# Performance work log

Measured on AMD Instinct MI355X. Metric: run time of the kernel, lower is better.

## Reference

```python
import jax, jax.numpy as jnp
import numpy as np

LENS = 4.0
SCALE = 0.25
NUM_HEADS = 16


def _multispike(u):
    # floor(clamp(u, 0, 4) + 0.5)
    return jnp.floor(jnp.clip(u, 0.0, 4.0) + 0.5)


def _ms_act(x):
    # Multispike module: spike(4*x) / 4
    return _multispike(4.0 * x) / 4.0


def setup_inputs() -> dict:
    key = jax.random.key(0)
    ks = jax.random.split(key, 5)
    N, D = 65536, 1024
    x = jax.random.normal(ks[0], (N, D), dtype=jnp.float32)
    s = 1.0 / np.sqrt(D)
    Wq = jax.random.normal(ks[1], (D, D), dtype=jnp.float32) * s
    Wk = jax.random.normal(ks[2], (D, D), dtype=jnp.float32) * s
    Wv = jax.random.normal(ks[3], (D, D), dtype=jnp.float32) * s
    Wp = jax.random.normal(ks[4], (D, D), dtype=jnp.float32) * s
    return {"x": x, "Wq": Wq, "Wk": Wk, "Wv": Wv, "Wp": Wp}


def reference(x, Wq, Wk, Wv, Wp):
    N, C = x.shape
    H = NUM_HEADS
    hd = C // H

    xs = _ms_act(x)
    q = _ms_act(xs @ Wq.T)  # [N, C]
    k = _ms_act(xs @ Wk.T)
    v = _ms_act(xs @ Wv.T)

    q = q.reshape(N, H, hd)
    k = k.reshape(N, H, hd)
    v = v.reshape(N, H, hd)

    # linear attention: kv = k^T @ v per head -> [H, hd, hd]
    kv = jnp.einsum('nhd,nhe->hde', k, v)
    attn = jnp.einsum('nhd,hde->nhe', q, kv) * SCALE  # [N, H, hd]
    attn = attn.reshape(N, C)
    return attn @ Wp.T
```

## Files before the change

kernel.cpp:

```cpp
#include <hip/hip_runtime.h>
#include <stdint.h>


typedef __attribute__((ext_vector_type(8))) __bf16 bf16x8;
typedef __attribute__((ext_vector_type(4))) float f32x4;

__device__ __forceinline__ float bf2f(unsigned short u) {
  return __builtin_bit_cast(float, (unsigned int)u << 16);
}
__device__ __forceinline__ unsigned short f2bf(float f) {
  unsigned int u = __builtin_bit_cast(unsigned int, f);
  u += 0x7FFFu + ((u >> 16) & 1u);
  return (unsigned short)(u >> 16);
}
__device__ __forceinline__ float ms_act(float x) {
  float t = fminf(fmaxf(4.0f * x, 0.0f), 4.0f);
  return floorf(t + 0.5f) * 0.25f;
}

#define GLD16(g, l)                                                                           \
  __builtin_amdgcn_global_load_lds((__attribute__((address_space(1))) void*)(const void*)(g), \
                                   (__attribute__((address_space(3))) void*)(l), 16, 0, 0)

__global__ __launch_bounds__(256) void split_w_kernel(
    const float* __restrict__ Wq, const float* __restrict__ Wk, const float* __restrict__ Wv,
    unsigned short* __restrict__ Whi, unsigned short* __restrict__ Wlo, float* __restrict__ kv) {
  const int tid = threadIdx.x;
  const int w = blockIdx.y;
  const float* W = (w == 0) ? Wq : (w == 1) ? Wk : Wv;
  const size_t base = (size_t)w * 1048576u;
  const size_t i = (size_t)(blockIdx.x * 256 + tid) * 4;
  float4 v = *(const float4*)&W[i];
  float vv[4] = {v.x, v.y, v.z, v.w};
  unsigned short h4[4], l4[4];
#pragma unroll
  for (int j = 0; j < 4; ++j) {
    unsigned short hi = f2bf(vv[j]);
    h4[j] = hi;
    l4[j] = f2bf(vv[j] - bf2f(hi));
  }
  *(uint2*)&Whi[base + i] = make_uint2((unsigned)h4[0] | ((unsigned)h4[1] << 16),
                                       (unsigned)h4[2] | ((unsigned)h4[3] << 16));
  *(uint2*)&Wlo[base + i] = make_uint2((unsigned)l4[0] | ((unsigned)l4[1] << 16),
                                       (unsigned)l4[2] | ((unsigned)l4[3] << 16));
  if (w == 0 && blockIdx.x < 64) {
    ((float4*)kv)[blockIdx.x * 256 + tid] = make_float4(0.f, 0.f, 0.f, 0.f);
  }
}

__global__ __launch_bounds__(256) void act_x_kernel(const float* __restrict__ x,
                                                    unsigned short* __restrict__ xs,
                                                    long long n4) {
  long long i = (long long)blockIdx.x * 256 + threadIdx.x;
  const long long stride = (long long)gridDim.x * 256;
  for (; i < n4; i += stride) {
    float4 v = ((const float4*)x)[i];
    unsigned int lo = (unsigned)f2bf(ms_act(v.x)) | ((unsigned)f2bf(ms_act(v.y)) << 16);
    unsigned int hi = (unsigned)f2bf(ms_act(v.z)) | ((unsigned)f2bf(ms_act(v.w)) << 16);
    ((uint2*)xs)[i] = make_uint2(lo, hi);
  }
}

template <int QUANT, int LOG_NCB>
__global__ __launch_bounds__(512, 2) void gemm8(const unsigned short* __restrict__ A, size_t lda,
                                                const unsigned short* __restrict__ Bh,
                                                const unsigned short* __restrict__ Bl,
                                                unsigned short* __restrict__ C0,
                                                unsigned short* __restrict__ C1,
                                                float* __restrict__ Cf) {
  extern __shared__ unsigned short smem[];
  unsigned short* sA = smem;
  unsigned short* sBh = smem + 32768;
  unsigned short* sBl = smem + 49152;

  constexpr int NCB = 1 << LOG_NCB;
  const int chunk = (int)gridDim.x >> 3;
  const int gid = blockIdx.x;
  const int g2 = (gid & 7) * chunk + (gid >> 3);
  const int rowb = g2 >> LOG_NCB;
  const int cb = g2 & (NCB - 1);
  const size_t rowBase = (size_t)rowb * 256;
  const int colBase = cb * 128;

  const int tid = threadIdx.x;
  const int lane = tid & 63;
  const int wid = tid >> 6;
  const int wm = wid >> 1;
  const int wn = wid & 1;
  const int r15 = lane & 15;
  const int ks = lane >> 4;

  const int rl0 = tid >> 2;
  const int sswz = (tid >> 3) & 3;
  const int scol = ((tid & 3) ^ sswz) << 3;
  const unsigned short* pA0 = A + (rowBase + rl0) * lda + scol;
  const unsigned short* pA1 = pA0 + 128 * lda;
  const unsigned short* pBh = Bh + ((size_t)(colBase + rl0)) * 1024 + scol;
  const unsigned short* pBl = Bl + ((size_t)(colBase + rl0)) * 1024 + scol;

  auto stage = [&](int t) {
    const int buf = t & 3;
    const int k0 = t * 32;
    GLD16(pA0 + k0, sA + buf * 8192 + tid * 8);
    GLD16(pA1 + k0, sA + buf * 8192 + 4096 + tid * 8);
    GLD16(pBh + k0, sBh + buf * 4096 + tid * 8);
    GLD16(pBl + k0, sBl + buf * 4096 + tid * 8);
  };

  const int slotr = (ks ^ ((r15 >> 1) & 3)) * 8;
  int offA[4], offB[4];
#pragma unroll
  for (int m = 0; m < 4; ++m) offA[m] = (wm * 64 + m * 16 + r15) * 32 + slotr;
#pragma unroll
  for (int n = 0; n < 4; ++n) offB[n] = (wn * 64 + n * 16 + r15) * 32 + slotr;

  f32x4 acc[4][4];
#pragma unroll
  for (int m = 0; m < 4; ++m)
#pragma unroll
    for (int n = 0; n < 4; ++n) acc[m][n] = (f32x4)(0.0f);

#define VMW(N) asm volatile("s_waitcnt vmcnt(" #N ")" ::: "memory")
#define PHASE(S, DOSTAGE)                                                                   \
  {                                                                                         \
    __syncthreads();                                                                        \
    if (DOSTAGE) stage((S) + 3);                                                            \
    const int buf = (S) & 3;                                                                \
    bf16x8 a[4], bh[4], bl[4];                                                              \
    _Pragma("unroll") for (int m = 0; m < 4; ++m)                                           \
        a[m] = *(const bf16x8*)&sA[buf * 8192 + offA[m]];                                   \
    _Pragma("unroll") for (int n = 0; n < 4; ++n) {                                         \
      bh[n] = *(const bf16x8*)&sBh[buf * 4096 + offB[n]];                                   \
      bl[n] = *(const bf16x8*)&sBl[buf * 4096 + offB[n]];                                   \
    }                                                                                       \
    asm volatile("s_waitcnt lgkmcnt(0)" ::: "memory");                                      \
    __builtin_amdgcn_sched_barrier(0);                                                      \
    __builtin_amdgcn_s_setprio(1);                                                          \
    _Pragma("unroll") for (int m = 0; m < 4; ++m)                                           \
      _Pragma("unroll") for (int n = 0; n < 4; ++n)                                         \
          acc[m][n] = __builtin_amdgcn_mfma_f32_16x16x32_bf16(a[m], bh[n], acc[m][n], 0, 0, 0); \
    _Pragma("unroll") for (int m = 0; m < 4; ++m)                                           \
      _Pragma("unroll") for (int n = 0; n < 4; ++n)                                         \
          acc[m][n] = __builtin_amdgcn_mfma_f32_16x16x32_bf16(a[m], bl[n], acc[m][n], 0, 0, 0); \
    __builtin_amdgcn_s_setprio(0);                                                          \
  }

  stage(0);
  stage(1);
  stage(2);
  for (int s = 0; s < 29; ++s) {
    VMW(8);
    PHASE(s, true);
  }
  VMW(8); PHASE(29, false);
  VMW(4); PHASE(30, false);
  VMW(0); PHASE(31, false);
#undef PHASE
#undef VMW

  const int rq = ks * 4;
  if (QUANT) {
    const int mat = colBase >> 10;
    unsigned short* Cq = mat ? C1 : C0;
    const int ccb = colBase & 1023;
#pragma unroll
    for (int m = 0; m < 4; ++m)
#pragma unroll
      for (int n = 0; n < 4; ++n) {
        const size_t row0 = rowBase + wm * 64 + m * 16 + rq;
        const int col = ccb + wn * 64 + n * 16 + r15;
#pragma unroll
        for (int j = 0; j < 4; ++j) Cq[(row0 + j) * 1024 + col] = f2bf(ms_act(acc[m][n][j]));
      }
  } else {
#pragma unroll
    for (int m = 0; m < 4; ++m)
#pragma unroll
      for (int n = 0; n < 4; ++n) {
        const size_t row0 = rowBase + wm * 64 + m * 16 + rq;
        const int col = colBase + wn * 64 + n * 16 + r15;
#pragma unroll
        for (int j = 0; j < 4; ++j) Cf[(row0 + j) * 1024 + col] = acc[m][n][j];
      }
  }
}

__global__ __launch_bounds__(256) void kv_kernel(const unsigned short* __restrict__ K,
                                                 const unsigned short* __restrict__ V,
                                                 float* __restrict__ kv) {
  const int h = blockIdx.x;
  const long long n0 = (long long)blockIdx.y * 1024;
  const int tid = threadIdx.x;
  __shared__ unsigned short kss[16 * 64];
  __shared__ unsigned short vs[16 * 64];
  float acc[4][4] = {};
  const int db = (tid >> 4) * 4;
  const int eb = (tid & 15) * 4;
  const int idx = tid * 4;
  const int nl = idx >> 6, c = idx & 63;
  for (int s = 0; s < 64; ++s) {
    const long long nrow = n0 + s * 16 + nl;
    *(uint2*)&kss[idx] = *(const uint2*)&K[nrow * 1024 + h * 64 + c];
    *(uint2*)&vs[idx] = *(const uint2*)&V[nrow * 1024 + h * 64 + c];
    __syncthreads();
#pragma unroll
    for (int t = 0; t < 16; ++t) {
      float kd[4], ve[4];
#pragma unroll
      for (int i = 0; i < 4; ++i) kd[i] = bf2f(kss[t * 64 + db + i]);
#pragma unroll
      for (int j = 0; j < 4; ++j) ve[j] = bf2f(vs[t * 64 + eb + j]);
#pragma unroll
      for (int i = 0; i < 4; ++i)
#pragma unroll
        for (int j = 0; j < 4; ++j) acc[i][j] += kd[i] * ve[j];
    }
    __syncthreads();
  }
  float* base = kv + h * 4096;
#pragma unroll
  for (int i = 0; i < 4; ++i)
#pragma unroll
    for (int j = 0; j < 4; ++j) atomicAdd(&base[(db + i) * 64 + eb + j], acc[i][j]);
}

__global__ __launch_bounds__(256) void u_kernel(const float* __restrict__ kv,
                                                const float* __restrict__ Wp,
                                                unsigned short* __restrict__ Uhi,
                                                unsigned short* __restrict__ Ulo) {
  const int h = blockIdx.x;
  const int jb = blockIdx.y;
  const int tid = threadIdx.x;
  __shared__ float kvs[64 * 64];
  __shared__ float wps[64 * 64];
#pragma unroll
  for (int r = 0; r < 4; ++r) {
    const int f = tid + r * 256;
    ((float4*)kvs)[f] = ((const float4*)(kv + h * 4096))[f];
    ((float4*)wps)[f] =
        *(const float4*)&Wp[(size_t)(jb * 64 + (f >> 4)) * 1024 + h * 64 + (f & 15) * 4];
  }
  __syncthreads();
  const int db = (tid >> 4) * 4;
  const int jl = (tid & 15) * 4;
  float acc[4][4] = {};
  for (int e = 0; e < 64; ++e) {
    float kd[4], wj[4];
#pragma unroll
    for (int i = 0; i < 4; ++i) kd[i] = kvs[(db + i) * 64 + e];
#pragma unroll
    for (int j = 0; j < 4; ++j) wj[j] = wps[(jl + j) * 64 + e];
#pragma unroll
    for (int i = 0; i < 4; ++i)
#pragma unroll
      for (int j = 0; j < 4; ++j) acc[i][j] += kd[i] * wj[j];
  }
#pragma unroll
  for (int j = 0; j < 4; ++j)
#pragma unroll
    for (int i = 0; i < 4; ++i) {
      const float u = acc[i][j] * 0.25f;
      const unsigned short hi = f2bf(u);
      const unsigned short lo = f2bf(u - bf2f(hi));
      const size_t off = (size_t)(jb * 64 + jl + j) * 1024 + h * 64 + db + i;
      Uhi[off] = hi;
      Ulo[off] = lo;
    }
}

extern "C" void kernel_launch(void* const* d_in, const int* in_sizes, int n_in,
                              void* d_out, int out_size, void* d_ws, size_t ws_size,
                              hipStream_t stream) {
  const float* x = (const float*)d_in[0];
  const float* Wq = (const float*)d_in[1];
  const float* Wk = (const float*)d_in[2];
  const float* Wv = (const float*)d_in[3];
  const float* Wp = (const float*)d_in[4];
  float* out = (float*)d_out;

  char* ws = (char*)d_ws;
  const size_t NC2 = 134217728ull;
  unsigned short* xs = (unsigned short*)(ws);
  unsigned short* bufA = (unsigned short*)(ws + NC2);
  unsigned short* bufB = (unsigned short*)(ws + 2 * NC2);
  unsigned short* Whi = (unsigned short*)(ws + 3 * NC2);
  unsigned short* Wlo = Whi + 3ull * 1048576;
  float* kvb = (float*)(ws + 3 * NC2 + 12582912ull);
  unsigned short* Uhi = (unsigned short*)(ws + 3 * NC2 + 12582912ull + 262144ull);
  unsigned short* Ulo = Uhi + 1048576;

  hipFuncSetAttribute((const void*)gemm8<1, 4>, hipFuncAttributeMaxDynamicSharedMemorySize,
                      131072);
  hipFuncSetAttribute((const void*)gemm8<1, 3>, hipFuncAttributeMaxDynamicSharedMemorySize,
                      131072);
  hipFuncSetAttribute((const void*)gemm8<0, 3>, hipFuncAttributeMaxDynamicSharedMemorySize,
                      131072);

  dim3 blk(256);
  split_w_kernel<<<dim3(1024, 3), blk, 0, stream>>>(Wq, Wk, Wv, Whi, Wlo, kvb);
  act_x_kernel<<<2048, blk, 0, stream>>>(x, xs, 16777216LL);
  gemm8<1, 4><<<4096, 512, 131072, stream>>>(xs, 1024, Whi + 1048576, Wlo + 1048576, bufA, bufB,
                                             nullptr);
  kv_kernel<<<dim3(16, 64), blk, 0, stream>>>(bufA, bufB, kvb);
  gemm8<1, 3><<<2048, 512, 131072, stream>>>(xs, 1024, Whi, Wlo, bufA, bufA, nullptr);
  u_kernel<<<dim3(16, 16), blk, 0, stream>>>(kvb, Wp, Uhi, Ulo);
  gemm8<0, 3><<<2048, 512, 131072, stream>>>(bufA, 1024, Uhi, Ulo, nullptr, nullptr, out);
}
```

Baseline: 1.734 ms.

## Interleave hi/lo weight split along K and widen GEMM tile to 256x256

```diff
diff --git a/kernel.cpp b/kernel.cpp
--- a/kernel.cpp
+++ b/kernel.cpp
@@ -24,13 +24,15 @@
 
 __global__ __launch_bounds__(256) void split_w_kernel(
     const float* __restrict__ Wq, const float* __restrict__ Wk, const float* __restrict__ Wv,
-    unsigned short* __restrict__ Whi, unsigned short* __restrict__ Wlo, float* __restrict__ kv) {
+    unsigned short* __restrict__ W2, float* __restrict__ kv) {
   const int tid = threadIdx.x;
   const int w = blockIdx.y;
   const float* W = (w == 0) ? Wq : (w == 1) ? Wk : Wv;
-  const size_t base = (size_t)w * 1048576u;
-  const size_t i = (size_t)(blockIdx.x * 256 + tid) * 4;
-  float4 v = *(const float4*)&W[i];
+  unsigned short* P = W2 + (size_t)w * 2097152u;
+  const int idx = blockIdx.x * 256 + tid;
+  const int row = idx >> 8;
+  const int c0 = (idx & 255) * 4;
+  float4 v = *(const float4*)&W[(size_t)row * 1024 + c0];
   float vv[4] = {v.x, v.y, v.z, v.w};
   unsigned short h4[4], l4[4];
 #pragma unroll
@@ -39,10 +41,10 @@
     h4[j] = hi;
     l4[j] = f2bf(vv[j] - bf2f(hi));
   }
-  *(uint2*)&Whi[base + i] = make_uint2((unsigned)h4[0] | ((unsigned)h4[1] << 16),
-                                       (unsigned)h4[2] | ((unsigned)h4[3] << 16));
-  *(uint2*)&Wlo[base + i] = make_uint2((unsigned)l4[0] | ((unsigned)l4[1] << 16),
-                                       (unsigned)l4[2] | ((unsigned)l4[3] << 16));
+  *(uint2*)&P[(size_t)row * 2048 + c0] =
+      make_uint2((unsigned)h4[0] | ((unsigned)h4[1] << 16), (unsigned)h4[2] | ((unsigned)h4[3] << 16));
+  *(uint2*)&P[(size_t)row * 2048 + 1024 + c0] =
+      make_uint2((unsigned)l4[0] | ((unsigned)l4[1] << 16), (unsigned)l4[2] | ((unsigned)l4[3] << 16));
   if (w == 0 && blockIdx.x < 64) {
     ((float4*)kv)[blockIdx.x * 256 + tid] = make_float4(0.f, 0.f, 0.f, 0.f);
   }
@@ -62,16 +64,14 @@
 }
 
 template <int QUANT, int LOG_NCB>
-__global__ __launch_bounds__(512, 2) void gemm8(const unsigned short* __restrict__ A, size_t lda,
-                                                const unsigned short* __restrict__ Bh,
-                                                const unsigned short* __restrict__ Bl,
+__global__ __launch_bounds__(512, 2) void gemm8(const unsigned short* __restrict__ A,
+                                                const unsigned short* __restrict__ B2,
                                                 unsigned short* __restrict__ C0,
                                                 unsigned short* __restrict__ C1,
                                                 float* __restrict__ Cf) {
   extern __shared__ unsigned short smem[];
   unsigned short* sA = smem;
-  unsigned short* sBh = smem + 32768;
-  unsigned short* sBl = smem + 49152;
+  unsigned short* sB = smem + 32768;
 
   constexpr int NCB = 1 << LOG_NCB;
   const int chunk = (int)gridDim.x >> 3;
@@ -80,104 +80,122 @@
   const int rowb = g2 >> LOG_NCB;
   const int cb = g2 & (NCB - 1);
   const size_t rowBase = (size_t)rowb * 256;
-  const int colBase = cb * 128;
+  const int colBase = cb * 256;
 
   const int tid = threadIdx.x;
   const int lane = tid & 63;
   const int wid = tid >> 6;
-  const int wm = wid >> 1;
-  const int wn = wid & 1;
+  const int wm = wid >> 2;
+  const int wn = wid & 3;
   const int r15 = lane & 15;
   const int ks = lane >> 4;
 
   const int rl0 = tid >> 2;
   const int sswz = (tid >> 3) & 3;
   const int scol = ((tid & 3) ^ sswz) << 3;
-  const unsigned short* pA0 = A + (rowBase + rl0) * lda + scol;
-  const unsigned short* pA1 = pA0 + 128 * lda;
-  const unsigned short* pBh = Bh + ((size_t)(colBase + rl0)) * 1024 + scol;
-  const unsigned short* pBl = Bl + ((size_t)(colBase + rl0)) * 1024 + scol;
-
-  auto stage = [&](int t) {
-    const int buf = t & 3;
-    const int k0 = t * 32;
-    GLD16(pA0 + k0, sA + buf * 8192 + tid * 8);
-    GLD16(pA1 + k0, sA + buf * 8192 + 4096 + tid * 8);
-    GLD16(pBh + k0, sBh + buf * 4096 + tid * 8);
-    GLD16(pBl + k0, sBl + buf * 4096 + tid * 8);
+  const unsigned short* pA0 = A + (rowBase + rl0) * 1024 + scol;
+  const unsigned short* pA1 = pA0 + 128 * 1024;
+  const unsigned short* pB0 = B2 + (size_t)(colBase + rl0) * 2048 + scol;
+  const unsigned short* pB1 = pB0 + 128 * 2048;
+  const int ldst = tid * 8;
+
+  auto stage_a = [&](int t) {
+    const int buf = (t & 3) * 8192;
+    const int ka = (t * 32) & 1023;
+    GLD16(pA0 + ka, sA + buf + ldst);
+    GLD16(pA1 + ka, sA + buf + 4096 + ldst);
   };
+  auto stage_b = [&](int t) {
+    const int buf = (t & 3) * 8192;
+    const int kb = t * 32;
+    GLD16(pB0 + kb, sB + buf + ldst);
+    GLD16(pB1 + kb, sB + buf + 4096 + ldst);
+  };
 
   const int slotr = (ks ^ ((r15 >> 1) & 3)) * 8;
-  int offA[4], offB[4];
-#pragma unroll
-  for (int m = 0; m < 4; ++m) offA[m] = (wm * 64 + m * 16 + r15) * 32 + slotr;
+  int offA[8], offB[4];
+#pragma unroll
+  for (int m = 0; m < 8; ++m) offA[m] = (wm * 128 + m * 16 + r15) * 32 + slotr;
 #pragma unroll
   for (int n = 0; n < 4; ++n) offB[n] = (wn * 64 + n * 16 + r15) * 32 + slotr;
 
-  f32x4 acc[4][4];
-#pragma unroll
-  for (int m = 0; m < 4; ++m)
+  f32x4 acc[8][4];
+#pragma unroll
+  for (int m = 0; m < 8; ++m)
 #pragma unroll
     for (int n = 0; n < 4; ++n) acc[m][n] = (f32x4)(0.0f);
 
 #define VMW(N) asm volatile("s_waitcnt vmcnt(" #N ")" ::: "memory")
-#define PHASE(S, DOSTAGE)                                                                   \
-  {                                                                                         \
-    __syncthreads();                                                                        \
-    if (DOSTAGE) stage((S) + 3);                                                            \
-    const int buf = (S) & 3;                                                                \
-    bf16x8 a[4], bh[4], bl[4];                                                              \
-    _Pragma("unroll") for (int m = 0; m < 4; ++m)                                           \
-        a[m] = *(const bf16x8*)&sA[buf * 8192 + offA[m]];                                   \
-    _Pragma("unroll") for (int n = 0; n < 4; ++n) {                                         \
-      bh[n] = *(const bf16x8*)&sBh[buf * 4096 + offB[n]];                                   \
-      bl[n] = *(const bf16x8*)&sBl[buf * 4096 + offB[n]];                                   \
-    }                                                                                       \
-    asm volatile("s_waitcnt lgkmcnt(0)" ::: "memory");                                      \
-    __builtin_amdgcn_sched_barrier(0);                                                      \
-    __builtin_amdgcn_s_setprio(1);                                                          \
-    _Pragma("unroll") for (int m = 0; m < 4; ++m)                                           \
-      _Pragma("unroll") for (int n = 0; n < 4; ++n)                                         \
-          acc[m][n] = __builtin_amdgcn_mfma_f32_16x16x32_bf16(a[m], bh[n], acc[m][n], 0, 0, 0); \
-    _Pragma("unroll") for (int m = 0; m < 4; ++m)                                           \
-      _Pragma("unroll") for (int n = 0; n < 4; ++n)                                         \
-          acc[m][n] = __builtin_amdgcn_mfma_f32_16x16x32_bf16(a[m], bl[n], acc[m][n], 0, 0, 0); \
-    __builtin_amdgcn_s_setprio(0);                                                          \
-  }
-
-  stage(0);
-  stage(1);
-  stage(2);
-  for (int s = 0; s < 29; ++s) {
-    VMW(8);
-    PHASE(s, true);
-  }
-  VMW(8); PHASE(29, false);
-  VMW(4); PHASE(30, false);
-  VMW(0); PHASE(31, false);
-#undef PHASE
+#define SLAB(S, WN, DS)                                                                          \
+  {                                                                                              \
+    VMW(WN);                     \
+    __builtin_amdgcn_s_barrier();                                                                \
+    asm volatile("" ::: "memory");                                                               \
+    if (DS) stage_a((S) + 3);                                                                    \
+    const int buf_ = ((S)&3) * 8192;                                                             \
+    bf16x8 bfr[4];                                                                               \
+    _Pragma("unroll") for (int n = 0; n < 4; ++n) bfr[n] =                                       \
+        *(const bf16x8*)&sB[buf_ + offB[n]];                                                     \
+    {                                                                                            \
+      bf16x8 aP[4];                                                                              \
+      _Pragma("unroll") for (int mi = 0; mi < 4; ++mi) aP[mi] =                                  \
+          *(const bf16x8*)&sA[buf_ + offA[mi]];                                                  \
+      asm volatile("s_waitcnt lgkmcnt(0)" ::: "memory");                                         \
+      __builtin_amdgcn_sched_barrier(0);                                                         \
+      __builtin_amdgcn_s_setprio(1);                                                             \
+      _Pragma("unroll") for (int mi = 0; mi < 4; ++mi) _Pragma("unroll") for (int n = 0; n < 4;  \
+                                                                              ++n) acc[mi][n] =  \
+          __builtin_amdgcn_mfma_f32_16x16x32_bf16(aP[mi], bfr[n], acc[mi][n], 0, 0, 0);          \
+      __builtin_amdgcn_s_setprio(0);                                                             \
+    }                                                                                            \
+    if (DS) stage_b((S) + 3);                                                                    \
+    {                                                                                            \
+      bf16x8 aP[4];                                                                              \
+      _Pragma("unroll") for (int mi = 0; mi < 4; ++mi) aP[mi] =                                  \
+          *(const bf16x8*)&sA[buf_ + offA[4 + mi]];                                              \
+      asm volatile("s_waitcnt lgkmcnt(0)" ::: "memory");                                         \
+      __builtin_amdgcn_sched_barrier(0);                                                         \
+      __builtin_amdgcn_s_setprio(1);                                                             \
+      _Pragma("unroll") for (int mi = 0; mi < 4; ++mi) _Pragma("unroll") for (int n = 0; n < 4;  \
+                                                                              ++n)               \
+          acc[4 + mi][n] =                                                                       \
+          __builtin_amdgcn_mfma_f32_16x16x32_bf16(aP[mi], bfr[n], acc[4 + mi][n], 0, 0, 0);      \
+      __builtin_amdgcn_s_setprio(0);                                                             \
+    }                                                                                            \
+  }
+
+  stage_a(0); stage_b(0);
+  stage_a(1); stage_b(1);
+  stage_a(2); stage_b(2);
+  for (int s = 0; s < 61; ++s) {
+    SLAB(s, 8, true);
+  }
+  SLAB(61, 8, false);
+  SLAB(62, 4, false);
+  SLAB(63, 0, false);
+#undef SLAB
 #undef VMW
 
   const int rq = ks * 4;
   if (QUANT) {
     const int mat = colBase >> 10;
     unsigned short* Cq = mat ? C1 : C0;
-    const int ccb = colBase & 1023;
-#pragma unroll
-    for (int m = 0; m < 4; ++m)
+    const int cb0 = (colBase & 1023) + wn * 64;
+#pragma unroll
+    for (int m = 0; m < 8; ++m)
 #pragma unroll
       for (int n = 0; n < 4; ++n) {
-        const size_t row0 = rowBase + wm * 64 + m * 16 + rq;
-        const int col = ccb + wn * 64 + n * 16 + r15;
+        const size_t row0 = rowBase + wm * 128 + m * 16 + rq;
+        const int col = cb0 + n * 16 + r15;
 #pragma unroll
         for (int j = 0; j < 4; ++j) Cq[(row0 + j) * 1024 + col] = f2bf(ms_act(acc[m][n][j]));
       }
   } else {
 #pragma unroll
-    for (int m = 0; m < 4; ++m)
+    for (int m = 0; m < 8; ++m)
 #pragma unroll
       for (int n = 0; n < 4; ++n) {
-        const size_t row0 = rowBase + wm * 64 + m * 16 + rq;
+        const size_t row0 = rowBase + wm * 128 + m * 16 + rq;
         const int col = colBase + wn * 64 + n * 16 + r15;
 #pragma unroll
         for (int j = 0; j < 4; ++j) Cf[(row0 + j) * 1024 + col] = acc[m][n][j];
@@ -226,8 +244,7 @@
 
 __global__ __launch_bounds__(256) void u_kernel(const float* __restrict__ kv,
                                                 const float* __restrict__ Wp,
-                                                unsigned short* __restrict__ Uhi,
-                                                unsigned short* __restrict__ Ulo) {
+                                                unsigned short* __restrict__ U2) {
   const int h = blockIdx.x;
   const int jb = blockIdx.y;
   const int tid = threadIdx.x;
@@ -262,9 +279,9 @@
       const float u = acc[i][j] * 0.25f;
       const unsigned short hi = f2bf(u);
       const unsigned short lo = f2bf(u - bf2f(hi));
-      const size_t off = (size_t)(jb * 64 + jl + j) * 1024 + h * 64 + db + i;
-      Uhi[off] = hi;
-      Ulo[off] = lo;
+      const size_t off = (size_t)(jb * 64 + jl + j) * 2048 + h * 64 + db + i;
+      U2[off] = hi;
+      U2[off + 1024] = lo;
     }
 }
 
@@ -283,26 +300,23 @@
   unsigned short* xs = (unsigned short*)(ws);
   unsigned short* bufA = (unsigned short*)(ws + NC2);
   unsigned short* bufB = (unsigned short*)(ws + 2 * NC2);
-  unsigned short* Whi = (unsigned short*)(ws + 3 * NC2);
-  unsigned short* Wlo = Whi + 3ull * 1048576;
+  unsigned short* W2 = (unsigned short*)(ws + 3 * NC2);
   float* kvb = (float*)(ws + 3 * NC2 + 12582912ull);
-  unsigned short* Uhi = (unsigned short*)(ws + 3 * NC2 + 12582912ull + 262144ull);
-  unsigned short* Ulo = Uhi + 1048576;
-
-  hipFuncSetAttribute((const void*)gemm8<1, 4>, hipFuncAttributeMaxDynamicSharedMemorySize,
-                      131072);
+  unsigned short* U2 = (unsigned short*)(ws + 3 * NC2 + 12582912ull + 262144ull);
+
   hipFuncSetAttribute((const void*)gemm8<1, 3>, hipFuncAttributeMaxDynamicSharedMemorySize,
                       131072);
-  hipFuncSetAttribute((const void*)gemm8<0, 3>, hipFuncAttributeMaxDynamicSharedMemorySize,
+  hipFuncSetAttribute((const void*)gemm8<1, 2>, hipFuncAttributeMaxDynamicSharedMemorySize,
                       131072);
+  hipFuncSetAttribute((const void*)gemm8<0, 2>, hipFuncAttributeMaxDynamicSharedMemorySize,
+                      131072);
 
   dim3 blk(256);
-  split_w_kernel<<<dim3(1024, 3), blk, 0, stream>>>(Wq, Wk, Wv, Whi, Wlo, kvb);
+  split_w_kernel<<<dim3(1024, 3), blk, 0, stream>>>(Wq, Wk, Wv, W2, kvb);
   act_x_kernel<<<2048, blk, 0, stream>>>(x, xs, 16777216LL);
-  gemm8<1, 4><<<4096, 512, 131072, stream>>>(xs, 1024, Whi + 1048576, Wlo + 1048576, bufA, bufB,
-                                             nullptr);
+  gemm8<1, 3><<<2048, 512, 131072, stream>>>(xs, W2 + 2097152, bufA, bufB, nullptr);
   kv_kernel<<<dim3(16, 64), blk, 0, stream>>>(bufA, bufB, kvb);
-  gemm8<1, 3><<<2048, 512, 131072, stream>>>(xs, 1024, Whi, Wlo, bufA, bufA, nullptr);
-  u_kernel<<<dim3(16, 16), blk, 0, stream>>>(kvb, Wp, Uhi, Ulo);
-  gemm8<0, 3><<<2048, 512, 131072, stream>>>(bufA, 1024, Uhi, Ulo, nullptr, nullptr, out);
-}
+  gemm8<1, 2><<<1024, 512, 131072, stream>>>(xs, W2, bufA, bufA, nullptr);
+  u_kernel<<<dim3(16, 16), blk, 0, stream>>>(kvb, Wp, U2);
+  gemm8<0, 2><<<1024, 512, 131072, stream>>>(bufA, U2, nullptr, nullptr, out);
+}
```

New measurement: 1.541 ms. -11.1%, faster.
